# Kernel tuning notes

Hardware: AMD Instinct MI355X
Metric: run time of the kernel (lower is better)

The kernel has to match this reference:

```python
import jax, jax.numpy as jnp
import numpy as np

NUM_EXPERTS = 8
TOP_K = 2


def setup_inputs() -> dict:
    key = jax.random.key(0)
    k0, k1, k2, k3, k4 = jax.random.split(key, 5)
    T, D, F, E = 4096, 2048, 4096, NUM_EXPERTS  # tokens, hidden, intermediate, experts
    s_in = 1.0 / np.sqrt(D).astype(np.float32)
    s_mid = 1.0 / np.sqrt(F).astype(np.float32)
    return {
        "hidden_states": jax.random.normal(k0, (T, D), jnp.float32),
        "gate_w": jax.random.normal(k1, (D, E), jnp.float32) * s_in,   # router gate (no bias)
        "w1": jax.random.normal(k2, (E, D, F), jnp.float32) * s_in,     # expert gate proj
        "w3": jax.random.normal(k3, (E, D, F), jnp.float32) * s_in,     # expert up proj
        "w2": jax.random.normal(k4, (E, F, D), jnp.float32) * s_mid,    # expert down proj
    }


def reference(hidden_states, gate_w, w1, w3, w2):
    x = hidden_states  # [T, D] (original flattens any leading dims)
    # Router: logits in fp32 (router_logits.float()), softmax over ALL experts,
    # take top-k WITHOUT renormalization (renormalize=False).
    logits = (x @ gate_w).astype(jnp.float32)            # [T, E]
    probs = jax.nn.softmax(logits, axis=-1)              # [T, E]
    topk_w, topk_i = jax.lax.top_k(probs, TOP_K)         # [T, K]
    # Dense combine weights: zero for non-selected experts. [T, E]
    combine = jnp.sum(
        jax.nn.one_hot(topk_i, NUM_EXPERTS, dtype=x.dtype) * topk_w[..., None],
        axis=1,
    )

    # SwiGLU experts, vmapped over the expert axis (fixed, small E).
    def expert_fn(w1e, w3e, w2e):
        return (jax.nn.silu(x @ w1e) * (x @ w3e)) @ w2e  # [T, D]

    expert_out = jax.vmap(expert_fn)(w1, w3, w2)         # [E, T, D]
    return jnp.einsum("te,etd->td", combine, expert_out)  # [T, D]
```

## Files before the change

kernel.cpp:

```cpp
#include <hip/hip_runtime.h>
#include <hip/hip_bf16.h>

#define TK 4096
#define DD 2048
#define FF 4096
#define NE 8
#define BM 128
#define BN 128
#define BK 64

typedef __attribute__((ext_vector_type(8))) short bf16x8;
typedef __attribute__((ext_vector_type(4))) short bf16x4;
typedef __attribute__((ext_vector_type(4))) float f32x4;

#define SWZ(r) ((((r) & 7) ^ (((r) >> 3) & 7)) << 4)

__device__ __forceinline__ unsigned short f2bf(float f) {
  unsigned u = __builtin_bit_cast(unsigned, f);
  return (unsigned short)((u + 0x7FFFu + ((u >> 16) & 1u)) >> 16);
}

__device__ __forceinline__ bf16x4 pack4(float a, float b, float c, float d) {
  bf16x4 r;
  r[0] = (short)f2bf(a); r[1] = (short)f2bf(b);
  r[2] = (short)f2bf(c); r[3] = (short)f2bf(d);
  return r;
}

__device__ __forceinline__ bf16x8 lds_frag(const unsigned short* base, int row, int kbyte) {
  int boff = (row * 128 + kbyte) ^ SWZ(row);
  return *(const bf16x8*)((const char*)base + boff);
}

__global__ void k_router(const float* __restrict__ x, const float* __restrict__ gw,
                         int* __restrict__ cnt, int* __restrict__ ltok,
                         float* __restrict__ lw) {
  int tok = (blockIdx.x * blockDim.x + threadIdx.x) >> 6;
  int lane = threadIdx.x & 63;
  if (tok >= TK) return;
  const float* xr = x + (size_t)tok * DD;
  float a0=0,a1=0,a2=0,a3=0,a4=0,a5=0,a6=0,a7=0;
  for (int p = 0; p < DD / 256; ++p) {
    int d0 = p * 256 + lane * 4;
    f32x4 xv = *(const f32x4*)(xr + d0);
#pragma unroll
    for (int j = 0; j < 4; ++j) {
      float xs = xv[j];
      const f32x4* g = (const f32x4*)(gw + (size_t)(d0 + j) * NE);
      f32x4 g0 = g[0], g1 = g[1];
      a0 += xs * g0[0]; a1 += xs * g0[1]; a2 += xs * g0[2]; a3 += xs * g0[3];
      a4 += xs * g1[0]; a5 += xs * g1[1]; a6 += xs * g1[2]; a7 += xs * g1[3];
    }
  }
#pragma unroll
  for (int s = 32; s > 0; s >>= 1) {
    a0 += __shfl_xor(a0, s, 64); a1 += __shfl_xor(a1, s, 64);
    a2 += __shfl_xor(a2, s, 64); a3 += __shfl_xor(a3, s, 64);
    a4 += __shfl_xor(a4, s, 64); a5 += __shfl_xor(a5, s, 64);
    a6 += __shfl_xor(a6, s, 64); a7 += __shfl_xor(a7, s, 64);
  }
  if (lane == 0) {
    float p_[NE] = {a0, a1, a2, a3, a4, a5, a6, a7};
    float m = p_[0];
#pragma unroll
    for (int e = 1; e < NE; ++e) m = fmaxf(m, p_[e]);
    float ssum = 0.f;
#pragma unroll
    for (int e = 0; e < NE; ++e) { p_[e] = __expf(p_[e] - m); ssum += p_[e]; }
    float inv = 1.f / ssum;
    int i1 = 0; float b1 = p_[0];
#pragma unroll
    for (int e = 1; e < NE; ++e) if (p_[e] > b1) { b1 = p_[e]; i1 = e; }
    int i2 = -1; float b2 = -1.f;
#pragma unroll
    for (int e = 0; e < NE; ++e) if (e != i1 && p_[e] > b2) { b2 = p_[e]; i2 = e; }
    int s1 = atomicAdd(&cnt[i1], 1);
    ltok[i1 * TK + s1] = tok; lw[i1 * TK + s1] = b1 * inv;
    int s2 = atomicAdd(&cnt[i2], 1);
    ltok[i2 * TK + s2] = tok; lw[i2 * TK + s2] = b2 * inv;
  }
}

__global__ void k_prefix(const int* __restrict__ cnt, int* __restrict__ off) {
  if (threadIdx.x == 0) {
    int a = 0;
#pragma unroll
    for (int e = 0; e < NE; ++e) { off[e] = a; a += cnt[e]; }
    off[NE] = a;
  }
}

__global__ __launch_bounds__(256, 2)
void k_gemm1(const float* __restrict__ x, const float* __restrict__ w1g,
             const float* __restrict__ w3g, const int* __restrict__ cnt,
             const int* __restrict__ off, const int* __restrict__ ltok,
             const float* __restrict__ lw, unsigned short* __restrict__ H) {
  const int e = blockIdx.z;
  const int ce = cnt[e];
  const int m0 = blockIdx.y * BM;
  if (m0 >= ce) return;
  const int n0 = blockIdx.x * BN;
  const int tid = threadIdx.x;
  const int lane = tid & 63;
  const int wv = tid >> 6;
  const int wr = wv >> 1, wc = wv & 1;
  const float* W1 = w1g + (size_t)e * DD * FF;
  const float* W3 = w3g + (size_t)e * DD * FF;
  const int base = off[e];

  __shared__ unsigned short As[BM * BK];
  __shared__ unsigned short B1s[BN * BK];
  __shared__ unsigned short B3s[BN * BK];

  const int arow = tid >> 1;
  const int ahalf = tid & 1;
  const int gmrow = m0 + arow;
  const float* xrow = (gmrow < ce) ? (x + (size_t)ltok[e * TK + gmrow] * DD) : nullptr;

  f32x4 acc1[4][4], acc3[4][4];
#pragma unroll
  for (int m = 0; m < 4; ++m)
#pragma unroll
    for (int n = 0; n < 4; ++n)
#pragma unroll
      for (int j = 0; j < 4; ++j) { acc1[m][n][j] = 0.f; acc3[m][n][j] = 0.f; }

  for (int kt = 0; kt < DD / BK; ++kt) {
    const int k0 = kt * BK;
    f32x4 av[8];
#pragma unroll
    for (int j = 0; j < 8; ++j) {
      if (xrow) av[j] = *(const f32x4*)(xrow + k0 + ahalf * 32 + j * 4);
      else { av[j][0] = 0.f; av[j][1] = 0.f; av[j][2] = 0.f; av[j][3] = 0.f; }
    }
    f32x4 w1v[2][4];
#pragma unroll
    for (int b = 0; b < 2; ++b) {
      const int bi = tid + (b << 8);
      const int dblk = bi >> 5, fblk = bi & 31;
      const float* p = W1 + (size_t)(k0 + dblk * 4) * FF + (n0 + fblk * 4);
#pragma unroll
      for (int r = 0; r < 4; ++r) w1v[b][r] = *(const f32x4*)(p + (size_t)r * FF);
    }
    __syncthreads();
#pragma unroll
    for (int j = 0; j < 8; ++j) {
      int boff = (arow * 128 + ahalf * 64 + j * 8) ^ SWZ(arow);
      *(bf16x4*)((char*)As + boff) = pack4(av[j][0], av[j][1], av[j][2], av[j][3]);
    }
#pragma unroll
    for (int b = 0; b < 2; ++b) {
      const int bi = tid + (b << 8);
      const int dblk = bi >> 5, fblk = bi & 31;
#pragma unroll
      for (int j = 0; j < 4; ++j) {
        int f = fblk * 4 + j;
        int boff = (f * 128 + dblk * 8) ^ SWZ(f);
        *(bf16x4*)((char*)B1s + boff) =
            pack4(w1v[0 + 0][0][j], w1v[b][1][j], w1v[b][2][j], w1v[b][3][j]);
        *(bf16x4*)((char*)B1s + boff) =
            pack4(w1v[b][0][j], w1v[b][1][j], w1v[b][2][j], w1v[b][3][j]);
      }
    }
    f32x4 w3v[2][4];
#pragma unroll
    for (int b = 0; b < 2; ++b) {
      const int bi = tid + (b << 8);
      const int dblk = bi >> 5, fblk = bi & 31;
      const float* p = W3 + (size_t)(k0 + dblk * 4) * FF + (n0 + fblk * 4);
#pragma unroll
      for (int r = 0; r < 4; ++r) w3v[b][r] = *(const f32x4*)(p + (size_t)r * FF);
    }
#pragma unroll
    for (int b = 0; b < 2; ++b) {
      const int bi = tid + (b << 8);
      const int dblk = bi >> 5, fblk = bi & 31;
#pragma unroll
      for (int j = 0; j < 4; ++j) {
        int f = fblk * 4 + j;
        int boff = (f * 128 + dblk * 8) ^ SWZ(f);
        *(bf16x4*)((char*)B3s + boff) =
            pack4(w3v[b][0][j], w3v[b][1][j], w3v[b][2][j], w3v[b][3][j]);
      }
    }
    __syncthreads();
#pragma unroll
    for (int kk = 0; kk < 2; ++kk) {
      const int kbyte = kk * 64 + (lane >> 4) * 16;
      bf16x8 af[4], b1f[4], b3f[4];
#pragma unroll
      for (int m = 0; m < 4; ++m) af[m] = lds_frag(As, wr * 64 + m * 16 + (lane & 15), kbyte);
#pragma unroll
      for (int n = 0; n < 4; ++n) {
        int row = wc * 64 + n * 16 + (lane & 15);
        b1f[n] = lds_frag(B1s, row, kbyte);
        b3f[n] = lds_frag(B3s, row, kbyte);
      }
#pragma unroll
      for (int m = 0; m < 4; ++m)
#pragma unroll
        for (int n = 0; n < 4; ++n) {
          acc1[m][n] = __builtin_amdgcn_mfma_f32_16x16x32_bf16(af[m], b1f[n], acc1[m][n], 0, 0, 0);
          acc3[m][n] = __builtin_amdgcn_mfma_f32_16x16x32_bf16(af[m], b3f[n], acc3[m][n], 0, 0, 0);
        }
    }
  }
#pragma unroll
  for (int m = 0; m < 4; ++m) {
    const int rbase = wr * 64 + m * 16 + ((lane >> 4) << 2);
    float wts[4]; bool val[4];
#pragma unroll
    for (int j = 0; j < 4; ++j) {
      int r = m0 + rbase + j;
      val[j] = r < ce;
      wts[j] = val[j] ? lw[e * TK + r] : 0.f;
    }
#pragma unroll
    for (int n = 0; n < 4; ++n) {
      const int col = n0 + wc * 64 + n * 16 + (lane & 15);
#pragma unroll
      for (int j = 0; j < 4; ++j) {
        if (!val[j]) continue;
        float s1 = acc1[m][n][j], s3 = acc3[m][n][j];
        float h = s1 / (1.f + __expf(-s1)) * s3 * wts[j];
        H[(size_t)(base + m0 + rbase + j) * FF + col] = f2bf(h);
      }
    }
  }
}

__global__ __launch_bounds__(256, 2)
void k_gemm2(const unsigned short* __restrict__ H, const float* __restrict__ w2g,
             const int* __restrict__ cnt, const int* __restrict__ off,
             const int* __restrict__ ltok, float* __restrict__ out) {
  const int e = blockIdx.z;
  const int ce = cnt[e];
  const int m0 = blockIdx.y * BM;
  if (m0 >= ce) return;
  const int n0 = blockIdx.x * BN;
  const int tid = threadIdx.x;
  const int lane = tid & 63;
  const int wv = tid >> 6;
  const int wr = wv >> 1, wc = wv & 1;
  const float* W2 = w2g + (size_t)e * FF * DD;
  const int base = off[e];

  __shared__ unsigned short As[BM * BK];
  __shared__ unsigned short Bs[BN * BK];

  const int arow = tid >> 1;
  const int ahalf = tid & 1;
  const bool aval = (m0 + arow) < ce;
  const unsigned short* hrow = H + (size_t)(base + m0 + arow) * FF;

  f32x4 acc[4][4];
#pragma unroll
  for (int m = 0; m < 4; ++m)
#pragma unroll
    for (int n = 0; n < 4; ++n)
#pragma unroll
      for (int j = 0; j < 4; ++j) acc[m][n][j] = 0.f;

  for (int kt = 0; kt < FF / BK; ++kt) {
    const int k0 = kt * BK;
    bf16x8 av[4];
#pragma unroll
    for (int j = 0; j < 4; ++j) {
      if (aval) av[j] = *(const bf16x8*)(hrow + k0 + ahalf * 32 + j * 8);
      else {
#pragma unroll
        for (int q = 0; q < 8; ++q) av[j][q] = 0;
      }
    }
    f32x4 wvv[2][4];
#pragma unroll
    for (int b = 0; b < 2; ++b) {
      const int bi = tid + (b << 8);
      const int kblk = bi >> 5, nblk = bi & 31;
      const float* p = W2 + (size_t)(k0 + kblk * 4) * DD + (n0 + nblk * 4);
#pragma unroll
      for (int r = 0; r < 4; ++r) wvv[b][r] = *(const f32x4*)(p + (size_t)r * DD);
    }
    __syncthreads();
#pragma unroll
    for (int j = 0; j < 4; ++j) {
      int boff = (arow * 128 + ahalf * 64 + j * 16) ^ SWZ(arow);
      *(bf16x8*)((char*)As + boff) = av[j];
    }
#pragma unroll
    for (int b = 0; b < 2; ++b) {
      const int bi = tid + (b << 8);
      const int kblk = bi >> 5, nblk = bi & 31;
#pragma unroll
      for (int j = 0; j < 4; ++j) {
        int f = nblk * 4 + j;
        int boff = (f * 128 + kblk * 8) ^ SWZ(f);
        *(bf16x4*)((char*)Bs + boff) =
            pack4(wvv[b][0][j], wvv[b][1][j], wvv[b][2][j], wvv[b][3][j]);
      }
    }
    __syncthreads();
#pragma unroll
    for (int kk = 0; kk < 2; ++kk) {
      const int kbyte = kk * 64 + (lane >> 4) * 16;
      bf16x8 af[4], bf[4];
#pragma unroll
      for (int m = 0; m < 4; ++m) af[m] = lds_frag(As, wr * 64 + m * 16 + (lane & 15), kbyte);
#pragma unroll
      for (int n = 0; n < 4; ++n) bf[n] = lds_frag(Bs, wc * 64 + n * 16 + (lane & 15), kbyte);
#pragma unroll
      for (int m = 0; m < 4; ++m)
#pragma unroll
        for (int n = 0; n < 4; ++n)
          acc[m][n] = __builtin_amdgcn_mfma_f32_16x16x32_bf16(af[m], bf[n], acc[m][n], 0, 0, 0);
    }
  }
#pragma unroll
  for (int m = 0; m < 4; ++m) {
    const int rbase = wr * 64 + m * 16 + ((lane >> 4) << 2);
    int toks[4]; bool val[4];
#pragma unroll
    for (int j = 0; j < 4; ++j) {
      int r = m0 + rbase + j;
      val[j] = r < ce;
      toks[j] = val[j] ? ltok[e * TK + r] : 0;
    }
#pragma unroll
    for (int n = 0; n < 4; ++n) {
      const int col = n0 + wc * 64 + n * 16 + (lane & 15);
#pragma unroll
      for (int j = 0; j < 4; ++j)
        if (val[j]) atomicAdd(out + (size_t)toks[j] * DD + col, acc[m][n][j]);
    }
  }
}

extern "C" void kernel_launch(void* const* d_in, const int* in_sizes, int n_in,
                              void* d_out, int out_size, void* d_ws, size_t ws_size,
                              hipStream_t stream) {
  const float* x  = (const float*)d_in[0];
  const float* gw = (const float*)d_in[1];
  const float* w1 = (const float*)d_in[2];
  const float* w3 = (const float*)d_in[3];
  const float* w2 = (const float*)d_in[4];
  float* out = (float*)d_out;

  char* ws = (char*)d_ws;
  int*   cnt  = (int*)(ws);
  int*   off  = (int*)(ws + 64);
  int*   ltok = (int*)(ws + 256);
  float* lw   = (float*)(ws + 256 + (size_t)NE * TK * 4);
  unsigned short* H = (unsigned short*)(ws + (1 << 20));
  const size_t need = (1u << 20) + (size_t)2 * TK * FF * 2;
  if (ws_size < need) return;

  hipMemsetAsync(cnt, 0, 64, stream);
  hipMemsetAsync(d_out, 0, (size_t)out_size * 4, stream);
  k_router<<<dim3(TK / 4), 256, 0, stream>>>(x, gw, cnt, ltok, lw);
  k_prefix<<<dim3(1), 64, 0, stream>>>(cnt, off);
  k_gemm1<<<dim3(FF / BN, TK / BM, NE), 256, 0, stream>>>(x, w1, w3, cnt, off, ltok, lw, H);
  k_gemm2<<<dim3(DD / BN, TK / BM, NE), 256, 0, stream>>>(H, w2, cnt, off, ltok, out);
}
```

Measured before the change: 1.119 ms.

## Double-buffer LDS tiles with register prefetch and halve K tile

Both expert GEMM kernels now use two LDS buffers per operand. The next K tile is loaded into registers before the compute of the current one, and written to the other buffer afterwards, so each iteration needs one barrier instead of two. BK drops from 64 to 32 to keep LDS within budget, the swizzle is rewritten for 64-byte rows, and the fp32-to-bf16 conversion now uses the library intrinsic. Global latency should overlap with MFMA work, at the cost of twice as many loop iterations and less work per barrier.

```diff
diff --git a/kernel.cpp b/kernel.cpp
--- a/kernel.cpp
+++ b/kernel.cpp
@@ -7,29 +7,28 @@
 #define NE 8
 #define BM 128
 #define BN 128
-#define BK 64
+#define BK 32
 
 typedef __attribute__((ext_vector_type(8))) short bf16x8;
 typedef __attribute__((ext_vector_type(4))) short bf16x4;
 typedef __attribute__((ext_vector_type(4))) float f32x4;
 
-#define SWZ(r) ((((r) & 7) ^ (((r) >> 3) & 7)) << 4)
-
 __device__ __forceinline__ unsigned short f2bf(float f) {
-  unsigned u = __builtin_bit_cast(unsigned, f);
-  return (unsigned short)((u + 0x7FFFu + ((u >> 16) & 1u)) >> 16);
-}
-
-__device__ __forceinline__ bf16x4 pack4(float a, float b, float c, float d) {
-  bf16x4 r;
-  r[0] = (short)f2bf(a); r[1] = (short)f2bf(b);
-  r[2] = (short)f2bf(c); r[3] = (short)f2bf(d);
-  return r;
-}
-
-__device__ __forceinline__ bf16x8 lds_frag(const unsigned short* base, int row, int kbyte) {
-  int boff = (row * 128 + kbyte) ^ SWZ(row);
-  return *(const bf16x8*)((const char*)base + boff);
+  return __builtin_bit_cast(unsigned short, __float2bfloat16(f));
+}
+
+__device__ __forceinline__ int swzoff(int row, int bir) {
+  int slot = (bir >> 4) ^ ((row & 3) ^ ((row >> 2) & 3));
+  return row * 64 + (slot << 4) + (bir & 15);
+}
+__device__ __forceinline__ bf16x8 frag(const unsigned short* base, int row, int kbyte) {
+  return *(const bf16x8*)((const char*)base + swzoff(row, kbyte));
+}
+__device__ __forceinline__ void put8(unsigned short* b, int row, int bir, bf16x4 v) {
+  *(bf16x4*)((char*)b + swzoff(row, bir)) = v;
+}
+__device__ __forceinline__ void put16(unsigned short* b, int row, int bir, bf16x8 v) {
+  *(bf16x8*)((char*)b + swzoff(row, bir)) = v;
 }
 
 __global__ void k_router(const float* __restrict__ x, const float* __restrict__ gw,
@@ -100,22 +99,19 @@
   const int m0 = blockIdx.y * BM;
   if (m0 >= ce) return;
   const int n0 = blockIdx.x * BN;
-  const int tid = threadIdx.x;
-  const int lane = tid & 63;
-  const int wv = tid >> 6;
+  const int tid = threadIdx.x, lane = tid & 63, wv = tid >> 6;
   const int wr = wv >> 1, wc = wv & 1;
   const float* W1 = w1g + (size_t)e * DD * FF;
   const float* W3 = w3g + (size_t)e * DD * FF;
   const int base = off[e];
 
-  __shared__ unsigned short As[BM * BK];
-  __shared__ unsigned short B1s[BN * BK];
-  __shared__ unsigned short B3s[BN * BK];
-
-  const int arow = tid >> 1;
-  const int ahalf = tid & 1;
-  const int gmrow = m0 + arow;
-  const float* xrow = (gmrow < ce) ? (x + (size_t)ltok[e * TK + gmrow] * DD) : nullptr;
+  __shared__ unsigned short As[2][BM * BK];
+  __shared__ unsigned short B1s[2][BN * BK];
+  __shared__ unsigned short B3s[2][BN * BK];
+
+  const int arow = tid >> 1, ah = tid & 1;
+  const float* xrow = (m0 + arow < ce) ? (x + (size_t)ltok[e * TK + (m0 + arow)] * DD) : nullptr;
+  const int dblk = tid >> 5, fblk = tid & 31;
 
   f32x4 acc1[4][4], acc3[4][4];
 #pragma unroll
@@ -125,86 +121,69 @@
 #pragma unroll
       for (int j = 0; j < 4; ++j) { acc1[m][n][j] = 0.f; acc3[m][n][j] = 0.f; }
 
-  for (int kt = 0; kt < DD / BK; ++kt) {
+  f32x4 av[4], v1[4], v3[4];
+
+  auto LOAD = [&](int kt) {
     const int k0 = kt * BK;
-    f32x4 av[8];
-#pragma unroll
-    for (int j = 0; j < 8; ++j) {
-      if (xrow) av[j] = *(const f32x4*)(xrow + k0 + ahalf * 32 + j * 4);
+#pragma unroll
+    for (int j = 0; j < 4; ++j) {
+      if (xrow) av[j] = *(const f32x4*)(xrow + k0 + ah * 16 + j * 4);
       else { av[j][0] = 0.f; av[j][1] = 0.f; av[j][2] = 0.f; av[j][3] = 0.f; }
     }
-    f32x4 w1v[2][4];
-#pragma unroll
-    for (int b = 0; b < 2; ++b) {
-      const int bi = tid + (b << 8);
-      const int dblk = bi >> 5, fblk = bi & 31;
-      const float* p = W1 + (size_t)(k0 + dblk * 4) * FF + (n0 + fblk * 4);
-#pragma unroll
-      for (int r = 0; r < 4; ++r) w1v[b][r] = *(const f32x4*)(p + (size_t)r * FF);
-    }
+    const float* p1 = W1 + (size_t)(k0 + dblk * 4) * FF + (n0 + fblk * 4);
+    const float* p3 = W3 + (size_t)(k0 + dblk * 4) * FF + (n0 + fblk * 4);
+#pragma unroll
+    for (int r = 0; r < 4; ++r) {
+      v1[r] = *(const f32x4*)(p1 + (size_t)r * FF);
+      v3[r] = *(const f32x4*)(p3 + (size_t)r * FF);
+    }
+  };
+  auto STORE = [&](int buf) {
+#pragma unroll
+    for (int j = 0; j < 4; ++j) {
+      bf16x4 t;
+      t[0] = (short)f2bf(av[j][0]); t[1] = (short)f2bf(av[j][1]);
+      t[2] = (short)f2bf(av[j][2]); t[3] = (short)f2bf(av[j][3]);
+      put8(As[buf], arow, ah * 32 + j * 8, t);
+    }
+#pragma unroll
+    for (int j = 0; j < 4; ++j) {
+      bf16x4 t1, t3;
+      t1[0] = (short)f2bf(v1[0][j]); t1[1] = (short)f2bf(v1[1][j]);
+      t1[2] = (short)f2bf(v1[2][j]); t1[3] = (short)f2bf(v1[3][j]);
+      t3[0] = (short)f2bf(v3[0][j]); t3[1] = (short)f2bf(v3[1][j]);
+      t3[2] = (short)f2bf(v3[2][j]); t3[3] = (short)f2bf(v3[3][j]);
+      put8(B1s[buf], fblk * 4 + j, dblk * 8, t1);
+      put8(B3s[buf], fblk * 4 + j, dblk * 8, t3);
+    }
+  };
+
+  LOAD(0);
+  STORE(0);
+  int cur = 0;
+  const int NT = DD / BK;
+  for (int kt = 0; kt < NT; ++kt) {
+    if (kt + 1 < NT) LOAD(kt + 1);
     __syncthreads();
-#pragma unroll
-    for (int j = 0; j < 8; ++j) {
-      int boff = (arow * 128 + ahalf * 64 + j * 8) ^ SWZ(arow);
-      *(bf16x4*)((char*)As + boff) = pack4(av[j][0], av[j][1], av[j][2], av[j][3]);
-    }
-#pragma unroll
-    for (int b = 0; b < 2; ++b) {
-      const int bi = tid + (b << 8);
-      const int dblk = bi >> 5, fblk = bi & 31;
-#pragma unroll
-      for (int j = 0; j < 4; ++j) {
-        int f = fblk * 4 + j;
-        int boff = (f * 128 + dblk * 8) ^ SWZ(f);
-        *(bf16x4*)((char*)B1s + boff) =
-            pack4(w1v[0 + 0][0][j], w1v[b][1][j], w1v[b][2][j], w1v[b][3][j]);
-        *(bf16x4*)((char*)B1s + boff) =
-            pack4(w1v[b][0][j], w1v[b][1][j], w1v[b][2][j], w1v[b][3][j]);
+    const int kb = (lane >> 4) * 16;
+    bf16x8 af[4];
+#pragma unroll
+    for (int m = 0; m < 4; ++m) af[m] = frag(As[cur], wr * 64 + m * 16 + (lane & 15), kb);
+#pragma unroll
+    for (int n = 0; n < 4; ++n) {
+      const int brow = wc * 64 + n * 16 + (lane & 15);
+      bf16x8 b1 = frag(B1s[cur], brow, kb);
+      bf16x8 b3 = frag(B3s[cur], brow, kb);
+#pragma unroll
+      for (int m = 0; m < 4; ++m) {
+        acc1[m][n] = __builtin_amdgcn_mfma_f32_16x16x32_bf16(af[m], b1, acc1[m][n], 0, 0, 0);
+        acc3[m][n] = __builtin_amdgcn_mfma_f32_16x16x32_bf16(af[m], b3, acc3[m][n], 0, 0, 0);
       }
     }
-    f32x4 w3v[2][4];
-#pragma unroll
-    for (int b = 0; b < 2; ++b) {
-      const int bi = tid + (b << 8);
-      const int dblk = bi >> 5, fblk = bi & 31;
-      const float* p = W3 + (size_t)(k0 + dblk * 4) * FF + (n0 + fblk * 4);
-#pragma unroll
-      for (int r = 0; r < 4; ++r) w3v[b][r] = *(const f32x4*)(p + (size_t)r * FF);
-    }
-#pragma unroll
-    for (int b = 0; b < 2; ++b) {
-      const int bi = tid + (b << 8);
-      const int dblk = bi >> 5, fblk = bi & 31;
-#pragma unroll
-      for (int j = 0; j < 4; ++j) {
-        int f = fblk * 4 + j;
-        int boff = (f * 128 + dblk * 8) ^ SWZ(f);
-        *(bf16x4*)((char*)B3s + boff) =
-            pack4(w3v[b][0][j], w3v[b][1][j], w3v[b][2][j], w3v[b][3][j]);
-      }
-    }
-    __syncthreads();
-#pragma unroll
-    for (int kk = 0; kk < 2; ++kk) {
-      const int kbyte = kk * 64 + (lane >> 4) * 16;
-      bf16x8 af[4], b1f[4], b3f[4];
-#pragma unroll
-      for (int m = 0; m < 4; ++m) af[m] = lds_frag(As, wr * 64 + m * 16 + (lane & 15), kbyte);
-#pragma unroll
-      for (int n = 0; n < 4; ++n) {
-        int row = wc * 64 + n * 16 + (lane & 15);
-        b1f[n] = lds_frag(B1s, row, kbyte);
-        b3f[n] = lds_frag(B3s, row, kbyte);
-      }
-#pragma unroll
-      for (int m = 0; m < 4; ++m)
-#pragma unroll
-        for (int n = 0; n < 4; ++n) {
-          acc1[m][n] = __builtin_amdgcn_mfma_f32_16x16x32_bf16(af[m], b1f[n], acc1[m][n], 0, 0, 0);
-          acc3[m][n] = __builtin_amdgcn_mfma_f32_16x16x32_bf16(af[m], b3f[n], acc3[m][n], 0, 0, 0);
-        }
-    }
-  }
+    if (kt + 1 < NT) STORE(cur ^ 1);
+    cur ^= 1;
+  }
+
 #pragma unroll
   for (int m = 0; m < 4; ++m) {
     const int rbase = wr * 64 + m * 16 + ((lane >> 4) << 2);
@@ -238,20 +217,18 @@
   const int m0 = blockIdx.y * BM;
   if (m0 >= ce) return;
   const int n0 = blockIdx.x * BN;
-  const int tid = threadIdx.x;
-  const int lane = tid & 63;
-  const int wv = tid >> 6;
+  const int tid = threadIdx.x, lane = tid & 63, wv = tid >> 6;
   const int wr = wv >> 1, wc = wv & 1;
   const float* W2 = w2g + (size_t)e * FF * DD;
   const int base = off[e];
 
-  __shared__ unsigned short As[BM * BK];
-  __shared__ unsigned short Bs[BN * BK];
-
-  const int arow = tid >> 1;
-  const int ahalf = tid & 1;
+  __shared__ unsigned short As[2][BM * BK];
+  __shared__ unsigned short Bs[2][BN * BK];
+
+  const int arow = tid >> 1, ah = tid & 1;
   const bool aval = (m0 + arow) < ce;
   const unsigned short* hrow = H + (size_t)(base + m0 + arow) * FF;
+  const int kblk = tid >> 5, nblk = tid & 31;
 
   f32x4 acc[4][4];
 #pragma unroll
@@ -261,60 +238,57 @@
 #pragma unroll
       for (int j = 0; j < 4; ++j) acc[m][n][j] = 0.f;
 
-  for (int kt = 0; kt < FF / BK; ++kt) {
+  bf16x8 av2[2];
+  f32x4 wv2[4];
+
+  auto LOAD = [&](int kt) {
     const int k0 = kt * BK;
-    bf16x8 av[4];
-#pragma unroll
-    for (int j = 0; j < 4; ++j) {
-      if (aval) av[j] = *(const bf16x8*)(hrow + k0 + ahalf * 32 + j * 8);
+#pragma unroll
+    for (int j = 0; j < 2; ++j) {
+      if (aval) av2[j] = *(const bf16x8*)(hrow + k0 + ah * 16 + j * 8);
       else {
 #pragma unroll
-        for (int q = 0; q < 8; ++q) av[j][q] = 0;
+        for (int q = 0; q < 8; ++q) av2[j][q] = 0;
       }
     }
-    f32x4 wvv[2][4];
-#pragma unroll
-    for (int b = 0; b < 2; ++b) {
-      const int bi = tid + (b << 8);
-      const int kblk = bi >> 5, nblk = bi & 31;
-      const float* p = W2 + (size_t)(k0 + kblk * 4) * DD + (n0 + nblk * 4);
-#pragma unroll
-      for (int r = 0; r < 4; ++r) wvv[b][r] = *(const f32x4*)(p + (size_t)r * DD);
-    }
+    const float* p = W2 + (size_t)(k0 + kblk * 4) * DD + (n0 + nblk * 4);
+#pragma unroll
+    for (int r = 0; r < 4; ++r) wv2[r] = *(const f32x4*)(p + (size_t)r * DD);
+  };
+  auto STORE = [&](int buf) {
+#pragma unroll
+    for (int j = 0; j < 2; ++j) put16(As[buf], arow, ah * 32 + j * 16, av2[j]);
+#pragma unroll
+    for (int j = 0; j < 4; ++j) {
+      bf16x4 t;
+      t[0] = (short)f2bf(wv2[0][j]); t[1] = (short)f2bf(wv2[1][j]);
+      t[2] = (short)f2bf(wv2[2][j]); t[3] = (short)f2bf(wv2[3][j]);
+      put8(Bs[buf], nblk * 4 + j, kblk * 8, t);
+    }
+  };
+
+  LOAD(0);
+  STORE(0);
+  int cur = 0;
+  const int NT = FF / BK;
+  for (int kt = 0; kt < NT; ++kt) {
+    if (kt + 1 < NT) LOAD(kt + 1);
     __syncthreads();
-#pragma unroll
-    for (int j = 0; j < 4; ++j) {
-      int boff = (arow * 128 + ahalf * 64 + j * 16) ^ SWZ(arow);
-      *(bf16x8*)((char*)As + boff) = av[j];
-    }
-#pragma unroll
-    for (int b = 0; b < 2; ++b) {
-      const int bi = tid + (b << 8);
-      const int kblk = bi >> 5, nblk = bi & 31;
-#pragma unroll
-      for (int j = 0; j < 4; ++j) {
-        int f = nblk * 4 + j;
-        int boff = (f * 128 + kblk * 8) ^ SWZ(f);
-        *(bf16x4*)((char*)Bs + boff) =
-            pack4(wvv[b][0][j], wvv[b][1][j], wvv[b][2][j], wvv[b][3][j]);
-      }
-    }
-    __syncthreads();
-#pragma unroll
-    for (int kk = 0; kk < 2; ++kk) {
-      const int kbyte = kk * 64 + (lane >> 4) * 16;
-      bf16x8 af[4], bf[4];
-#pragma unroll
-      for (int m = 0; m < 4; ++m) af[m] = lds_frag(As, wr * 64 + m * 16 + (lane & 15), kbyte);
-#pragma unroll
-      for (int n = 0; n < 4; ++n) bf[n] = lds_frag(Bs, wc * 64 + n * 16 + (lane & 15), kbyte);
+    const int kb = (lane >> 4) * 16;
+    bf16x8 af[4];
+#pragma unroll
+    for (int m = 0; m < 4; ++m) af[m] = frag(As[cur], wr * 64 + m * 16 + (lane & 15), kb);
+#pragma unroll
+    for (int n = 0; n < 4; ++n) {
+      bf16x8 bf = frag(Bs[cur], wc * 64 + n * 16 + (lane & 15), kb);
 #pragma unroll
       for (int m = 0; m < 4; ++m)
-#pragma unroll
-        for (int n = 0; n < 4; ++n)
-          acc[m][n] = __builtin_amdgcn_mfma_f32_16x16x32_bf16(af[m], bf[n], acc[m][n], 0, 0, 0);
-    }
-  }
+        acc[m][n] = __builtin_amdgcn_mfma_f32_16x16x32_bf16(af[m], bf, acc[m][n], 0, 0, 0);
+    }
+    if (kt + 1 < NT) STORE(cur ^ 1);
+    cur ^= 1;
+  }
+
 #pragma unroll
   for (int m = 0; m < 4; ++m) {
     const int rbase = wr * 64 + m * 16 + ((lane >> 4) << 2);
```

Result: faster. 979.1 us (-12.5%).
